# Kernel optimization log

Hardware: AMD Instinct MI355X
Metric: run time of the kernel (lower is better)

The kernel has to match this reference:

```python
import jax, jax.numpy as jnp
import numpy as np

EPS = 1e-4      # MovingBatchNorm eps
STEPS = 3       # fixed RK4 steps standing in for adaptive dopri5
B, N, D, C, H = 4, 2048, 3, 64, 512


def setup_inputs() -> dict:
    key = jax.random.key(0)
    ks = iter(jax.random.split(key, 40))
    f32 = jnp.float32

    def rn(shape, s=1.0):
        return jax.random.normal(next(ks), shape, dtype=f32) * s

    inp = {}
    inp['x'] = rn((B, N, D))
    inp['c'] = rn((B, N, C))
    for p in ('bn1', 'bn2'):
        inp[p + '_mean'] = rn((D,), 0.1)
        inp[p + '_var'] = jax.random.uniform(next(ks), (D,), dtype=f32, minval=0.5, maxval=1.5)
        inp[p + '_log_gamma'] = jnp.zeros((D,), f32)
        inp[p + '_beta'] = jnp.zeros((D,), f32)
    inp['sqrt_T'] = jnp.array([np.sqrt(0.5)], f32)  # train_T: T = sqrt_T**2
    dims = [(D, H), (H, H), (H, H), (H, D)]  # concatsquash (in, out)
    for i, (din, dout) in enumerate(dims):
        inp[f'W{i}'] = rn((dout, din), 0.05)
        inp[f'b{i}'] = jnp.zeros((dout,), f32)
        inp[f'Wg{i}'] = rn((dout, C + 1), 0.05)
        inp[f'bg{i}'] = jnp.zeros((dout,), f32)
        inp[f'Wb{i}'] = rn((dout, C + 1), 0.05)
    return inp


def _odenet(t, x, c, layers):
    # ConcatSquash MLP: lin(x)*sigmoid(hyper_gate([t,c])) + hyper_bias([t,c])
    ctx = jnp.concatenate([jnp.broadcast_to(t, c.shape[:-1] + (1,)).astype(x.dtype), c], axis=-1)
    h = x
    for i, (W, b, Wg, bg, Wb) in enumerate(layers):
        h = (h @ W.T + b) * jax.nn.sigmoid(ctx @ Wg.T + bg) + ctx @ Wb.T
        if i < len(layers) - 1:
            h = jnp.tanh(h)
    return h


def _aug_dyn(t, x, c, layers):
    # augmented CNF dynamics: (dx/dt, dlogp/dt) with exact divergence via D jvps
    f = lambda xx: _odenet(t, xx, c, layers)
    div = jnp.zeros(x.shape[:-1] + (1,), x.dtype)
    dx = None
    for i in range(x.shape[-1]):
        e = jnp.zeros_like(x).at[..., i].set(1.0)
        dx, jv = jax.jvp(f, (x,), (e,))
        div = div + jv[..., i:i + 1]
    return dx, -div


def _rk4(x0, lp0, c, layers, T):
    dt = T / STEPS

    def step(carry, i):
        x, lp = carry
        t = i.astype(x.dtype) * dt
        k1x, k1l = _aug_dyn(t, x, c, layers)
        k2x, k2l = _aug_dyn(t + 0.5 * dt, x + 0.5 * dt * k1x, c, layers)
        k3x, k3l = _aug_dyn(t + 0.5 * dt, x + 0.5 * dt * k2x, c, layers)
        k4x, k4l = _aug_dyn(t + dt, x + dt * k3x, c, layers)
        x = x + (dt / 6.0) * (k1x + 2.0 * k2x + 2.0 * k3x + k4x)
        lp = lp + (dt / 6.0) * (k1l + 2.0 * k2l + 2.0 * k3l + k4l)
        return (x, lp), None

    (x, lp), _ = jax.lax.scan(step, (x0, lp0), jnp.arange(STEPS))
    return x, lp


def _bn(x, lp, mean, var, log_gamma, beta):
    # MovingBatchNorm1d, eval mode; logdet = sum(log_gamma - 0.5*log(var+eps))
    y = (x - mean) * jnp.exp(log_gamma) / jnp.sqrt(var + EPS) + beta
    ld = jnp.sum(log_gamma - 0.5 * jnp.log(var + EPS))
    return y, lp - ld


def reference(x, c, bn1_mean, bn1_var, bn1_log_gamma, bn1_beta,
              bn2_mean, bn2_var, bn2_log_gamma, bn2_beta, sqrt_T,
              W0, b0, Wg0, bg0, Wb0, W1, b1, Wg1, bg1, Wb1,
              W2, b2, Wg2, bg2, Wb2, W3, b3, Wg3, bg3, Wb3):
    layers = [(W0, b0, Wg0, bg0, Wb0), (W1, b1, Wg1, bg1, Wb1),
              (W2, b2, Wg2, bg2, Wb2), (W3, b3, Wg3, bg3, Wb3)]
    lp = jnp.zeros(x.shape[:-1] + (1,), x.dtype)  # (B,N,1)
    x, lp = _bn(x, lp, bn1_mean, bn1_var, bn1_log_gamma, bn1_beta)
    T = sqrt_T[0] ** 2
    x, lp = _rk4(x, lp, c, layers, T)
    x, lp = _bn(x, lp, bn2_mean, bn2_var, bn2_log_gamma, bn2_beta)
    return x, jnp.sum(lp, axis=(1, 2))
```

## Files before the change

### kernel.cpp

```cpp
#include <hip/hip_runtime.h>
#include <hip/hip_fp8.h>

#define PTS 8192
#define HDIM 512
#define BN_EPS 1e-4f
#define HSTRB 528
#define TS 256.0f

typedef unsigned short u16;
typedef unsigned char u8;
typedef long long i64;
typedef u16 u16x8 __attribute__((ext_vector_type(8)));
typedef short s16x8 __attribute__((ext_vector_type(8)));
typedef float f32x4 __attribute__((ext_vector_type(4)));
typedef float f32x2 __attribute__((ext_vector_type(2)));

__device__ __forceinline__ float bf2f(u16 u) {
  unsigned x = ((unsigned)u) << 16;
  return __builtin_bit_cast(float, x);
}
__device__ __forceinline__ u16 f2bf(float f) {
  unsigned x = __builtin_bit_cast(unsigned, f);
  x += 0x7fffu + ((x >> 16) & 1u);
  return (u16)(x >> 16);
}
__device__ __forceinline__ u8 f2f8(float x) {
  int v = __builtin_amdgcn_cvt_pk_fp8_f32(x, x, 0, false);
  return (u8)(v & 0xff);
}
__device__ __forceinline__ unsigned pk4_f8(float a, float b, float c, float d) {
  int v = __builtin_amdgcn_cvt_pk_fp8_f32(a, b, 0, false);
  v = __builtin_amdgcn_cvt_pk_fp8_f32(c, d, v, true);
  return (unsigned)v;
}
__device__ __forceinline__ float sigf(float x) {
  return __builtin_amdgcn_rcpf(1.f + __expf(-x));
}
__device__ __forceinline__ float fast_tanh(float x) {
  float e = __expf(2.f * x);
  return 1.f - 2.f * __builtin_amdgcn_rcpf(e + 1.f);
}
__device__ __forceinline__ void gl2lds16(const u16* g, u16* l) {
  __builtin_amdgcn_global_load_lds(
      (const __attribute__((address_space(1))) void*)g,
      (__attribute__((address_space(3))) void*)l, 16, 0, 0);
}

struct PrepArgs {
  const float *W1, *W2;
  u8 *W1s, *W2s;
  const float* c;
  u16* cb;
  const float *Wg0, *Wg1, *Wg2, *Wb0, *Wb1, *Wb2;
  const float *bg0, *bg1, *bg2;
  u16* Wpack;
  float* bias_pack;
  const float *x, *m1, *v1, *lg1, *be1;
  float *x_cur, *lp_state;
  const float *Wg3, *bg3, *Wb3;
  float *G3, *B3;
  const float *W0, *b0, *b1, *b2, *W3;
  float *E0, *E1, *E2;
};
__global__ void prep_kernel(PrepArgs a) {
  int i = blockIdx.x * 256 + threadIdx.x;
  if (i < 512 * 512) {
    int n = i >> 9, k = i & 511;
    int c = k >> 5, kin = k & 31, q = kin >> 3, b = kin & 7;
    int w = n >> 6, nin = n & 63, j = nin >> 4, lr = nin & 15;
    size_t d = ((((size_t)(c * 8 + w) * 4 + j) * 64) + (q * 16 + lr)) * 8 + b;
    a.W1s[d] = f2f8(a.W1[i]);
    a.W2s[d] = f2f8(a.W2[i]);
  }
  if (i < PTS * 64) a.cb[i] = f2bf(a.c[i]);
  if (i < 6 * 512 * 64) {
    int sec = i >> 15;
    int within = i & 32767;
    int o = within >> 6, k = within & 63;
    const float* src[6] = {a.Wg0, a.Wg1, a.Wg2, a.Wb0, a.Wb1, a.Wb2};
    a.Wpack[i] = f2bf(src[sec][o * 65 + 1 + k]);
  }
  if (i < 3072) {
    int sec = i >> 9, o = i & 511;
    const float* bgl[3] = {a.bg0, a.bg1, a.bg2};
    a.bias_pack[i] = (sec < 3) ? bgl[sec][o] : 0.f;
  }
  if (i < 512) {
    int o = i;
    a.E0[o * 8 + 0] = a.W0[o * 3];
    a.E0[o * 8 + 1] = a.W0[o * 3 + 1];
    a.E0[o * 8 + 2] = a.W0[o * 3 + 2];
    a.E0[o * 8 + 3] = a.b0[o];
    a.E0[o * 8 + 4] = a.Wg0[o * 65];
    a.E0[o * 8 + 5] = a.Wb0[o * 65];
    a.E0[o * 8 + 6] = 0.f; a.E0[o * 8 + 7] = 0.f;
    a.E1[o * 4 + 0] = a.b1[o];
    a.E1[o * 4 + 1] = a.Wg1[o * 65];
    a.E1[o * 4 + 2] = a.Wb1[o * 65];
    a.E1[o * 4 + 3] = 0.f;
    a.E2[o * 8 + 0] = a.b2[o];
    a.E2[o * 8 + 1] = a.Wg2[o * 65];
    a.E2[o * 8 + 2] = a.Wb2[o * 65];
    a.E2[o * 8 + 3] = a.W3[o];
    a.E2[o * 8 + 4] = a.W3[512 + o];
    a.E2[o * 8 + 5] = a.W3[1024 + o];
    a.E2[o * 8 + 6] = 0.f; a.E2[o * 8 + 7] = 0.f;
  }
  if (i < PTS * 3) {
    int d = i % 3;
    a.x_cur[i] = (a.x[i] - a.m1[d]) * __expf(a.lg1[d]) * rsqrtf(a.v1[d] + BN_EPS) + a.be1[d];
  }
  if (i < PTS) a.lp_state[i] = 0.f;
  {
    int lane = threadIdx.x & 63;
    int p = (blockIdx.x * 256 + threadIdx.x) >> 6;
    float cv = a.c[(size_t)p * 64 + lane];
    float ag[3], ab[3];
    #pragma unroll
    for (int o = 0; o < 3; ++o) {
      ag[o] = cv * a.Wg3[o * 65 + 1 + lane];
      ab[o] = cv * a.Wb3[o * 65 + 1 + lane];
    }
    #pragma unroll
    for (int off = 32; off > 0; off >>= 1) {
      #pragma unroll
      for (int o = 0; o < 3; ++o) {
        ag[o] += __shfl_xor(ag[o], off);
        ab[o] += __shfl_xor(ab[o], off);
      }
    }
    if (lane == 0) {
      #pragma unroll
      for (int o = 0; o < 3; ++o) {
        a.G3[p * 3 + o] = ag[o] + a.bg3[o];
        a.B3[p * 3 + o] = ab[o];
      }
    }
  }
}

struct GatesGemmArgs {
  const u16 *A, *W;
  const float* bias;
  u16* GBi;
};
__global__ __launch_bounds__(256) void gates_gemm(GatesGemmArgs a) {
  __shared__ u16 As[128 * 32];
  __shared__ u16 Bs[128 * 32];
  int tid = threadIdx.x;
  int m0 = blockIdx.x * 128, n0 = blockIdx.y * 128;
  int wave = tid >> 6, lane = tid & 63;
  int wm = (wave & 1) * 64, wn = (wave >> 1) * 64;
  int lr = lane & 15, quad = lane >> 4;

  int rowS = tid >> 2, colS = (tid & 3) * 8;
  const u16* gA0 = a.A + (size_t)(m0 + rowS) * 64 + colS;
  const u16* gB0 = a.W + (size_t)(n0 + rowS) * 64 + colS;
  u16* sA0 = &As[tid * 8];
  u16* sA1 = &As[2048 + tid * 8];
  u16* sB0 = &Bs[tid * 8];
  u16* sB1 = &Bs[2048 + tid * 8];

  f32x4 acc[4][4];
  #pragma unroll
  for (int i = 0; i < 4; ++i)
    #pragma unroll
    for (int j = 0; j < 4; ++j)
      #pragma unroll
      for (int r = 0; r < 4; ++r) acc[i][j][r] = 0.f;

  for (int k0 = 0; k0 < 64; k0 += 32) {
    if (k0) __syncthreads();
    gl2lds16(gA0 + k0, sA0);
    gl2lds16(gA0 + (size_t)64 * 64 + k0, sA1);
    gl2lds16(gB0 + k0, sB0);
    gl2lds16(gB0 + (size_t)64 * 64 + k0, sB1);
    __syncthreads();
    s16x8 af[4], bfr[4];
    #pragma unroll
    for (int i = 0; i < 4; ++i)
      af[i] = *(const s16x8*)&As[(wm + i * 16 + lr) * 32 + quad * 8];
    #pragma unroll
    for (int j = 0; j < 4; ++j)
      bfr[j] = *(const s16x8*)&Bs[(wn + j * 16 + lr) * 32 + quad * 8];
    #pragma unroll
    for (int i = 0; i < 4; ++i)
      #pragma unroll
      for (int j = 0; j < 4; ++j)
        acc[i][j] = __builtin_amdgcn_mfma_f32_16x16x32_bf16(af[i], bfr[j], acc[i][j], 0, 0, 0);
  }

  #pragma unroll
  for (int j = 0; j < 4; ++j) {
    int n = n0 + wn + j * 16 + lr;
    int sec = n >> 9, col = n & 511;
    int l = (sec < 3) ? sec : sec - 3;
    int off = col * 2 + ((sec < 3) ? 0 : 1);
    float bv = a.bias[n];
    u16* outp = a.GBi + (size_t)l * PTS * 1024 + off;
    #pragma unroll
    for (int i = 0; i < 4; ++i) {
      int mrow = m0 + wm + i * 16 + quad * 4;
      #pragma unroll
      for (int r = 0; r < 4; ++r)
        outp[(size_t)(mrow + r) * 1024] = f2bf(acc[i][j][r] + bv);
    }
  }
}

struct StageArgs {
  const float* sqrtT;
  float ts_prev, ts_cur;
  int mode_prev;
  float* accum6;
  const float *G3, *B3, *Wg3, *Wb3, *b3;
  float *x_cur, *kx, *kl, *lp_state;
  const u16 *GBi0, *GBi1, *GBi2;
  const float *E0, *E1, *E2;
  const u8 *W1s, *W2s;
};

__global__ __launch_bounds__(512, 4) void stage_kernel(StageArgs a) {
  __shared__ __align__(16) u8 Hs[64 * HSTRB];
  __shared__ float xe[16][3];
  __shared__ float part[8][16][6];
  int tid = threadIdx.x;
  int w = tid >> 6, lane = tid & 63, lr = lane & 15, quad = lane >> 4;
  int n0 = w * 64;
  int p0 = blockIdx.x * 16;
  float s0 = a.sqrtT[0];
  float dt = s0 * s0 * (1.f / 3.f);

  const u8* w1l = a.W1s + (size_t)w * 2048 + (size_t)lane * 8;
  const u8* w2l = a.W2s + (size_t)w * 2048 + (size_t)lane * 8;

  i64 bc[4], bn[4];
  #pragma unroll
  for (int j = 0; j < 4; ++j) bc[j] = *(const i64*)(w1l + (size_t)j * 512);

  int pl0 = tid >> 5;
  int base_o = (tid & 31) * 16;
  const u16* g0row = a.GBi0 + (size_t)(p0 + pl0) * 1024 + 2 * base_o;
  u16x8 gc0 = *(const u16x8*)(g0row);
  u16x8 gc1 = *(const u16x8*)(g0row + 8);
  u16x8 gc2 = *(const u16x8*)(g0row + 16);
  u16x8 gc3 = *(const u16x8*)(g0row + 24);

  if (tid < 16) {
    int p = p0 + tid;
    float xc0 = a.x_cur[p * 3], xc1 = a.x_cur[p * 3 + 1], xc2 = a.x_cur[p * 3 + 2];
    float o0 = xc0, o1 = xc1, o2 = xc2;
    if (a.mode_prev >= 0) {
      float tp = a.ts_prev * dt;
      float dx[3], gate[3];
      #pragma unroll
      for (int r = 0; r < 3; ++r) {
        float fr = a.accum6[(size_t)p * 6 + r];
        gate[r] = sigf(a.G3[p * 3 + r] + tp * a.Wg3[r * 65]);
        float bias = a.B3[p * 3 + r] + tp * a.Wb3[r * 65];
        dx[r] = fmaf(fr + a.b3[r], gate[r], bias);
      }
      float klv = -(a.accum6[(size_t)p * 6 + 3] * gate[0] +
                    a.accum6[(size_t)p * 6 + 4] * gate[1] +
                    a.accum6[(size_t)p * 6 + 5] * gate[2]);
      int m = a.mode_prev;
      if (m == 0) {
        o0 = xc0 + 0.5f * dt * dx[0]; o1 = xc1 + 0.5f * dt * dx[1]; o2 = xc2 + 0.5f * dt * dx[2];
        a.kx[p * 3] = dx[0]; a.kx[p * 3 + 1] = dx[1]; a.kx[p * 3 + 2] = dx[2];
        a.kl[p] = klv;
      } else if (m == 1) {
        o0 = xc0 + 0.5f * dt * dx[0]; o1 = xc1 + 0.5f * dt * dx[1]; o2 = xc2 + 0.5f * dt * dx[2];
        a.kx[p * 3] += 2.f * dx[0]; a.kx[p * 3 + 1] += 2.f * dx[1]; a.kx[p * 3 + 2] += 2.f * dx[2];
        a.kl[p] += 2.f * klv;
      } else if (m == 2) {
        o0 = xc0 + dt * dx[0]; o1 = xc1 + dt * dx[1]; o2 = xc2 + dt * dx[2];
        a.kx[p * 3] += 2.f * dx[0]; a.kx[p * 3 + 1] += 2.f * dx[1]; a.kx[p * 3 + 2] += 2.f * dx[2];
        a.kl[p] += 2.f * klv;
      } else {
        float sc = dt * (1.f / 6.f);
        o0 = xc0 + sc * (a.kx[p * 3] + dx[0]);
        o1 = xc1 + sc * (a.kx[p * 3 + 1] + dx[1]);
        o2 = xc2 + sc * (a.kx[p * 3 + 2] + dx[2]);
        a.x_cur[p * 3] = o0; a.x_cur[p * 3 + 1] = o1; a.x_cur[p * 3 + 2] = o2;
        a.lp_state[p] += sc * (a.kl[p] + klv);
      }
    }
    xe[tid][0] = o0; xe[tid][1] = o1; xe[tid][2] = o2;
  }
  __syncthreads();

  float t = a.ts_cur * dt;

  {
    float x0 = xe[pl0][0], x1 = xe[pl0][1], x2 = xe[pl0][2];
    u16x8 gcv[4] = {gc0, gc1, gc2, gc3};
    #pragma unroll
    for (int cc = 0; cc < 4; ++cc) {
      u16x8 v = gcv[cc];
      float hk[4], d0k[4], d1k[4], d2k[4];
      #pragma unroll
      for (int k = 0; k < 4; ++k) {
        int o = base_o + cc * 4 + k;
        f32x4 e = *(const f32x4*)(a.E0 + (size_t)o * 8);
        f32x2 e2 = *(const f32x2*)(a.E0 + (size_t)o * 8 + 4);
        float u = fmaf(e[0], x0, fmaf(e[1], x1, e[2] * x2)) + e[3];
        float gate = sigf(bf2f(v[2 * k]) + t * e2[0]);
        float bias = bf2f(v[2 * k + 1]) + t * e2[1];
        float z = fmaf(u, gate, bias);
        float h = fast_tanh(z);
        float wm = (1.f - h * h) * gate * TS;
        hk[k] = h;
        d0k[k] = wm * e[0];
        d1k[k] = wm * e[1];
        d2k[k] = wm * e[2];
      }
      size_t hb = (size_t)(pl0 * 4) * HSTRB + base_o + cc * 4;
      *(unsigned*)(Hs + hb) = pk4_f8(hk[0], hk[1], hk[2], hk[3]);
      *(unsigned*)(Hs + hb + HSTRB) = pk4_f8(d0k[0], d0k[1], d0k[2], d0k[3]);
      *(unsigned*)(Hs + hb + 2 * HSTRB) = pk4_f8(d1k[0], d1k[1], d1k[2], d1k[3]);
      *(unsigned*)(Hs + hb + 3 * HSTRB) = pk4_f8(d2k[0], d2k[1], d2k[2], d2k[3]);
    }
  }

  unsigned g1v[4][4];
  #pragma unroll
  for (int j = 0; j < 4; ++j)
    #pragma unroll
    for (int i = 0; i < 4; ++i) {
      int n = n0 + j * 16 + lr;
      int p = p0 + i * 4 + quad;
      g1v[j][i] = *(const unsigned*)(a.GBi1 + (size_t)p * 1024 + 2 * n);
    }
  __syncthreads();

  f32x4 acc[4][4];
  #pragma unroll
  for (int i = 0; i < 4; ++i)
    #pragma unroll
    for (int j = 0; j < 4; ++j)
      #pragma unroll
      for (int r = 0; r < 4; ++r) acc[i][j][r] = 0.f;
  {
    #pragma unroll 1
    for (int c = 0; c < 16; ++c) {
      const u8* nsrc = (c < 15) ? (w1l + (size_t)(c + 1) * 16384) : w2l;
      #pragma unroll
      for (int j = 0; j < 4; ++j) bn[j] = *(const i64*)(nsrc + (size_t)j * 512);
      int k0 = c * 32;
      i64 af[4];
      #pragma unroll
      for (int i = 0; i < 4; ++i)
        af[i] = *(const i64*)(Hs + (size_t)(i * 16 + lr) * HSTRB + k0 + quad * 8);
      #pragma unroll
      for (int i = 0; i < 4; ++i)
        #pragma unroll
        for (int j = 0; j < 4; ++j)
          acc[i][j] = __builtin_amdgcn_mfma_f32_16x16x32_fp8_fp8(af[i], bc[j], acc[i][j], 0, 0, 0);
      #pragma unroll
      for (int j = 0; j < 4; ++j) bc[j] = bn[j];
    }
  }
  __syncthreads();

  #pragma unroll
  for (int j = 0; j < 4; ++j) {
    int n = n0 + j * 16 + lr;
    f32x4 e1 = *(const f32x4*)(a.E1 + (size_t)n * 4);
    #pragma unroll
    for (int i = 0; i < 4; ++i) {
      unsigned d = g1v[j][i];
      float gate = sigf(bf2f((u16)(d & 0xffffu)) + t * e1[1]);
      float bias = bf2f((u16)(d >> 16)) + t * e1[2];
      f32x4 u = acc[i][j];
      float z = fmaf(u[0] + e1[0], gate, bias);
      float h = fast_tanh(z);
      float wmf = (1.f - h * h) * gate;
      int row = i * 16 + quad * 4;
      Hs[(size_t)row * HSTRB + n] = f2f8(h);
      Hs[(size_t)(row + 1) * HSTRB + n] = f2f8(u[1] * wmf);
      Hs[(size_t)(row + 2) * HSTRB + n] = f2f8(u[2] * wmf);
      Hs[(size_t)(row + 3) * HSTRB + n] = f2f8(u[3] * wmf);
    }
  }

  unsigned g2v[4][4];
  #pragma unroll
  for (int j = 0; j < 4; ++j)
    #pragma unroll
    for (int i = 0; i < 4; ++i) {
      int n = n0 + j * 16 + lr;
      int p = p0 + i * 4 + quad;
      g2v[j][i] = *(const unsigned*)(a.GBi2 + (size_t)p * 1024 + 2 * n);
    }
  __syncthreads();

  #pragma unroll
  for (int i = 0; i < 4; ++i)
    #pragma unroll
    for (int j = 0; j < 4; ++j)
      #pragma unroll
      for (int r = 0; r < 4; ++r) acc[i][j][r] = 0.f;
  {
    #pragma unroll 1
    for (int c = 0; c < 16; ++c) {
      if (c < 15) {
        const u8* nsrc = w2l + (size_t)(c + 1) * 16384;
        #pragma unroll
        for (int j = 0; j < 4; ++j) bn[j] = *(const i64*)(nsrc + (size_t)j * 512);
      }
      int k0 = c * 32;
      i64 af[4];
      #pragma unroll
      for (int i = 0; i < 4; ++i)
        af[i] = *(const i64*)(Hs + (size_t)(i * 16 + lr) * HSTRB + k0 + quad * 8);
      #pragma unroll
      for (int i = 0; i < 4; ++i)
        #pragma unroll
        for (int j = 0; j < 4; ++j)
          acc[i][j] = __builtin_amdgcn_mfma_f32_16x16x32_fp8_fp8(af[i], bc[j], acc[i][j], 0, 0, 0);
      if (c < 15) {
        #pragma unroll
        for (int j = 0; j < 4; ++j) bc[j] = bn[j];
      }
    }
  }

  #pragma unroll
  for (int i = 0; i < 4; ++i) {
    float v0 = 0.f, v1 = 0.f, v2 = 0.f, v3 = 0.f, v4 = 0.f, v5 = 0.f;
    int pl = i * 4 + quad;
    #pragma unroll
    for (int j = 0; j < 4; ++j) {
      int n = n0 + j * 16 + lr;
      f32x4 ea = *(const f32x4*)(a.E2 + (size_t)n * 8);
      f32x2 eb = *(const f32x2*)(a.E2 + (size_t)n * 8 + 4);
      unsigned d = g2v[j][i];
      float gate = sigf(bf2f((u16)(d & 0xffffu)) + t * ea[1]);
      float bias = bf2f((u16)(d >> 16)) + t * ea[2];
      f32x4 u = acc[i][j];
      float z = fmaf(u[0] + ea[0], gate, bias);
      float h = fast_tanh(z);
      float wmf = (1.f - h * h) * gate;
      float w30 = ea[3], w31 = eb[0], w32 = eb[1];
      v0 = fmaf(h, w30, v0);
      v1 = fmaf(h, w31, v1);
      v2 = fmaf(h, w32, v2);
      v3 = fmaf(u[1] * wmf, w30, v3);
      v4 = fmaf(u[2] * wmf, w31, v4);
      v5 = fmaf(u[3] * wmf, w32, v5);
    }
    #pragma unroll
    for (int mask = 1; mask <= 8; mask <<= 1) {
      v0 += __shfl_xor(v0, mask);
      v1 += __shfl_xor(v1, mask);
      v2 += __shfl_xor(v2, mask);
      v3 += __shfl_xor(v3, mask);
      v4 += __shfl_xor(v4, mask);
      v5 += __shfl_xor(v5, mask);
    }
    float val = (lr == 0) ? v0 : (lr == 1) ? v1 : (lr == 2) ? v2
              : (lr == 3) ? v3 * (1.f / TS) : (lr == 4) ? v4 * (1.f / TS)
              : v5 * (1.f / TS);
    if (lr < 6) part[w][pl][lr] = val;
  }
  __syncthreads();

  if (tid < 96) {
    int pt = tid / 6, d = tid - pt * 6;
    float sum = 0.f;
    #pragma unroll
    for (int ww = 0; ww < 8; ++ww) sum += part[ww][pt][d];
    a.accum6[(size_t)(p0 + pt) * 6 + d] = sum;
  }
}

struct FinArgs {
  const float* sqrtT;
  const float* accum6;
  const float *G3, *B3, *Wg3, *Wb3, *b3;
  float *x_cur, *kx, *kl, *lp_state;
  const float *m2, *v2, *lg2, *be2;
  float* out_x;
};
__global__ void finalize_kernel(FinArgs a) {
  int p = blockIdx.x * 256 + threadIdx.x;
  if (p >= PTS) return;
  float s0 = a.sqrtT[0];
  float dt = s0 * s0 * (1.f / 3.f);
  float tp = 3.f * dt;
  float dx[3], gate[3];
  #pragma unroll
  for (int r = 0; r < 3; ++r) {
    float fr = a.accum6[(size_t)p * 6 + r];
    gate[r] = sigf(a.G3[p * 3 + r] + tp * a.Wg3[r * 65]);
    float bias = a.B3[p * 3 + r] + tp * a.Wb3[r * 65];
    dx[r] = fmaf(fr + a.b3[r], gate[r], bias);
  }
  float klv = -(a.accum6[(size_t)p * 6 + 3] * gate[0] +
                a.accum6[(size_t)p * 6 + 4] * gate[1] +
                a.accum6[(size_t)p * 6 + 5] * gate[2]);
  float sc = dt * (1.f / 6.f);
  #pragma unroll
  for (int r = 0; r < 3; ++r) {
    float xf = a.x_cur[p * 3 + r] + sc * (a.kx[p * 3 + r] + dx[r]);
    a.out_x[p * 3 + r] = (xf - a.m2[r]) * __expf(a.lg2[r]) * rsqrtf(a.v2[r] + BN_EPS) + a.be2[r];
  }
  a.lp_state[p] += sc * (a.kl[p] + klv);
}

__global__ void finish_lp(const float* __restrict__ lp_state,
                          const float* __restrict__ v1, const float* __restrict__ lg1,
                          const float* __restrict__ v2, const float* __restrict__ lg2,
                          float* __restrict__ out) {
  int b = blockIdx.x, tid = threadIdx.x;
  float s = 0.f;
  for (int n = tid; n < 2048; n += 256) s += lp_state[b * 2048 + n];
  __shared__ float red[256];
  red[tid] = s;
  __syncthreads();
  for (int w = 128; w > 0; w >>= 1) {
    if (tid < w) red[tid] += red[tid + w];
    __syncthreads();
  }
  if (tid == 0) {
    float ld = 0.f;
    for (int d = 0; d < 3; ++d) {
      ld += lg1[d] - 0.5f * logf(v1[d] + BN_EPS);
      ld += lg2[d] - 0.5f * logf(v2[d] + BN_EPS);
    }
    out[b] = red[0] - 2048.f * ld;
  }
}

extern "C" void kernel_launch(void* const* d_in, const int* in_sizes, int n_in,
                              void* d_out, int out_size, void* d_ws, size_t ws_size,
                              hipStream_t stream) {
  const float* x        = (const float*)d_in[0];
  const float* c        = (const float*)d_in[1];
  const float* bn1_mean = (const float*)d_in[2];
  const float* bn1_var  = (const float*)d_in[3];
  const float* bn1_lg   = (const float*)d_in[4];
  const float* bn1_beta = (const float*)d_in[5];
  const float* bn2_mean = (const float*)d_in[6];
  const float* bn2_var  = (const float*)d_in[7];
  const float* bn2_lg   = (const float*)d_in[8];
  const float* bn2_beta = (const float*)d_in[9];
  const float* sqrtT    = (const float*)d_in[10];
  const float* W0  = (const float*)d_in[11];
  const float* b0  = (const float*)d_in[12];
  const float* Wg0 = (const float*)d_in[13];
  const float* bg0 = (const float*)d_in[14];
  const float* Wb0 = (const float*)d_in[15];
  const float* W1  = (const float*)d_in[16];
  const float* b1  = (const float*)d_in[17];
  const float* Wg1 = (const float*)d_in[18];
  const float* bg1 = (const float*)d_in[19];
  const float* Wb1 = (const float*)d_in[20];
  const float* W2  = (const float*)d_in[21];
  const float* b2  = (const float*)d_in[22];
  const float* Wg2 = (const float*)d_in[23];
  const float* bg2 = (const float*)d_in[24];
  const float* Wb2 = (const float*)d_in[25];
  const float* W3  = (const float*)d_in[26];
  const float* b3  = (const float*)d_in[27];
  const float* Wg3 = (const float*)d_in[28];
  const float* bg3 = (const float*)d_in[29];
  const float* Wb3 = (const float*)d_in[30];

  char* base = (char*)d_ws;
  size_t off = 0;
  auto alloc = [&](size_t bytes) -> void* {
    void* pp = base + off;
    off += (bytes + 255) & ~(size_t)255;
    return pp;
  };
  u8* W1s = (u8*)alloc((size_t)512 * 512);
  u8* W2s = (u8*)alloc((size_t)512 * 512);
  u16* cb  = (u16*)alloc((size_t)PTS * 64 * 2);
  u16* Wpack = (u16*)alloc((size_t)6 * 512 * 64 * 2);
  float* bias_pack = (float*)alloc((size_t)3072 * 4);
  u16* GBi = (u16*)alloc((size_t)3 * PTS * 1024 * 2);
  const size_t SZi = (size_t)PTS * 1024;
  u16* GBi0 = GBi;
  u16* GBi1 = GBi + SZi;
  u16* GBi2 = GBi + 2 * SZi;
  float* G3f = (float*)alloc((size_t)PTS * 3 * 4);
  float* B3f = (float*)alloc((size_t)PTS * 3 * 4);
  float* E0 = (float*)alloc((size_t)512 * 8 * 4);
  float* E1 = (float*)alloc((size_t)512 * 4 * 4);
  float* E2 = (float*)alloc((size_t)512 * 8 * 4);
  float* accum6   = (float*)alloc((size_t)PTS * 6 * 4);
  float* x_cur    = (float*)alloc((size_t)PTS * 3 * 4);
  float* kx       = (float*)alloc((size_t)PTS * 3 * 4);
  float* kl       = (float*)alloc((size_t)PTS * 4);
  float* lp_state = (float*)alloc((size_t)PTS * 4);
  (void)ws_size; (void)in_sizes; (void)n_in; (void)out_size;

  PrepArgs pa{W1, W2, W1s, W2s, c, cb, Wg0, Wg1, Wg2, Wb0, Wb1, Wb2,
              bg0, bg1, bg2, Wpack, bias_pack, x, bn1_mean, bn1_var,
              bn1_lg, bn1_beta, x_cur, lp_state, Wg3, bg3, Wb3, G3f, B3f,
              W0, b0, b1, b2, W3, E0, E1, E2};
  prep_kernel<<<2048, 256, 0, stream>>>(pa);

  GatesGemmArgs gg{cb, Wpack, bias_pack, GBi};
  gates_gemm<<<dim3(64, 24), 256, 0, stream>>>(gg);

  auto ts_of = [](int s) -> float {
    static const float frac[4] = {0.f, 0.5f, 0.5f, 1.f};
    return (float)(s >> 2) + frac[s & 3];
  };

  for (int s = 0; s < 12; ++s) {
    StageArgs sa{sqrtT, (s == 0) ? 0.f : ts_of(s - 1), ts_of(s),
                 (s == 0) ? -1 : ((s - 1) & 3), accum6,
                 G3f, B3f, Wg3, Wb3, b3, x_cur, kx, kl, lp_state,
                 GBi0, GBi1, GBi2, E0, E1, E2, W1s, W2s};
    stage_kernel<<<PTS / 16, 512, 0, stream>>>(sa);
  }

  FinArgs fa{sqrtT, accum6, G3f, B3f, Wg3, Wb3, b3, x_cur, kx, kl,
             lp_state, bn2_mean, bn2_var, bn2_lg, bn2_beta, (float*)d_out};
  finalize_kernel<<<32, 256, 0, stream>>>(fa);
  finish_lp<<<4, 256, 0, stream>>>(lp_state, bn1_var, bn1_lg, bn2_var, bn2_lg,
                                   (float*)d_out + PTS * 3);
}
```

Before: 562.3 us.

## Fuse all RK4 stages into one persistent kernel using MX-scaled fp8 MFMA

Replaces the twelve stage launches and the finalize kernel with a single flow kernel. Each block keeps its 16 points' RK state (x, k-accumulators, logp) in shared memory across all 12 stages, which removes the per-stage global round-trips and launch gaps. The hidden-layer GEMMs switch from 16x16x32 fp8 MFMA to the scaled 16x16x128 f8f6f4 MFMA with unit scales, and W1/W2 are repacked to match, cutting instruction count per K chunk. In exchange, the persistent loop adds extra __syncthreads per stage, holds a larger register footprint for the 32-byte weight fragments, and re-reads the layer-0 gate data from global memory on every stage.

```diff
diff --git a/kernel.cpp b/kernel.cpp
--- a/kernel.cpp
+++ b/kernel.cpp
@@ -6,6 +6,7 @@
 #define BN_EPS 1e-4f
 #define HSTRB 528
 #define TS 256.0f
+#define SCL1 0x7f7f7f7f
 
 typedef unsigned short u16;
 typedef unsigned char u8;
@@ -14,6 +15,8 @@
 typedef short s16x8 __attribute__((ext_vector_type(8)));
 typedef float f32x4 __attribute__((ext_vector_type(4)));
 typedef float f32x2 __attribute__((ext_vector_type(2)));
+typedef int i32x4 __attribute__((ext_vector_type(4)));
+typedef int i32x8 __attribute__((ext_vector_type(8)));
 
 __device__ __forceinline__ float bf2f(u16 u) {
   unsigned x = ((unsigned)u) << 16;
@@ -56,7 +59,7 @@
   u16* Wpack;
   float* bias_pack;
   const float *x, *m1, *v1, *lg1, *be1;
-  float *x_cur, *lp_state;
+  float *x_cur;
   const float *Wg3, *bg3, *Wb3;
   float *G3, *B3;
   const float *W0, *b0, *b1, *b2, *W3;
@@ -66,9 +69,10 @@
   int i = blockIdx.x * 256 + threadIdx.x;
   if (i < 512 * 512) {
     int n = i >> 9, k = i & 511;
-    int c = k >> 5, kin = k & 31, q = kin >> 3, b = kin & 7;
-    int w = n >> 6, nin = n & 63, j = nin >> 4, lr = nin & 15;
-    size_t d = ((((size_t)(c * 8 + w) * 4 + j) * 64) + (q * 16 + lr)) * 8 + b;
+    int c = k >> 7, q2 = (k >> 5) & 3, b = k & 31;
+    int w = n >> 6, j = (n >> 4) & 3, lr = n & 15;
+    size_t d = (size_t)c * 65536 + (size_t)w * 8192 + (size_t)j * 2048 +
+               (size_t)(q2 * 16 + lr) * 32 + b;
     a.W1s[d] = f2f8(a.W1[i]);
     a.W2s[d] = f2f8(a.W2[i]);
   }
@@ -110,7 +114,6 @@
     int d = i % 3;
     a.x_cur[i] = (a.x[i] - a.m1[d]) * __expf(a.lg1[d]) * rsqrtf(a.v1[d] + BN_EPS) + a.be1[d];
   }
-  if (i < PTS) a.lp_state[i] = 0.f;
   {
     int lane = threadIdx.x & 63;
     int p = (blockIdx.x * 256 + threadIdx.x) >> 6;
@@ -208,22 +211,41 @@
   }
 }
 
-struct StageArgs {
+struct FlowArgs {
   const float* sqrtT;
-  float ts_prev, ts_cur;
-  int mode_prev;
-  float* accum6;
   const float *G3, *B3, *Wg3, *Wb3, *b3;
-  float *x_cur, *kx, *kl, *lp_state;
+  const float* x0;
   const u16 *GBi0, *GBi1, *GBi2;
   const float *E0, *E1, *E2;
   const u8 *W1s, *W2s;
+  const float *m2, *v2, *lg2, *be2;
+  float* out_x;
+  float* lp_state;
 };
 
-__global__ __launch_bounds__(512, 4) void stage_kernel(StageArgs a) {
+__device__ __forceinline__ void mx_chunk(const u8* hb, int c, f32x4 acc[4][4],
+                                         const i32x8 bw[4]) {
+  #pragma unroll
+  for (int i = 0; i < 4; ++i) {
+    const u8* ap = hb + (size_t)(i * 16) * HSTRB + c * 128;
+    i32x8 af;
+    *(i32x4*)&af = *(const i32x4*)ap;
+    *((i32x4*)&af + 1) = *(const i32x4*)(ap + 16);
+    #pragma unroll
+    for (int j = 0; j < 4; ++j)
+      acc[i][j] = __builtin_amdgcn_mfma_scale_f32_16x16x128_f8f6f4(
+          af, bw[j], acc[i][j], 0, 0, 0, SCL1, 0, SCL1);
+  }
+}
+
+__global__ __launch_bounds__(512, 4) void flow_kernel(FlowArgs a) {
   __shared__ __align__(16) u8 Hs[64 * HSTRB];
   __shared__ float xe[16][3];
   __shared__ float part[8][16][6];
+  __shared__ float xs[16][3], kxs[16][3];
+  __shared__ float kls[16], lps[16];
+  __shared__ float g3s[16][3], b3s[16][3];
+
   int tid = threadIdx.x;
   int w = tid >> 6, lane = tid & 63, lr = lane & 15, quad = lane >> 4;
   int n0 = w * 64;
@@ -231,281 +253,286 @@
   float s0 = a.sqrtT[0];
   float dt = s0 * s0 * (1.f / 3.f);
 
-  const u8* w1l = a.W1s + (size_t)w * 2048 + (size_t)lane * 8;
-  const u8* w2l = a.W2s + (size_t)w * 2048 + (size_t)lane * 8;
-
-  i64 bc[4], bn[4];
+  const u8* w1l = a.W1s + (size_t)w * 8192 + (size_t)lane * 32;
+  const u8* w2l = a.W2s + (size_t)w * 8192 + (size_t)lane * 32;
+  const u8* hb = (const u8*)Hs + (size_t)lr * HSTRB + quad * 32;
+
+  float wg3r[3], wb3r[3], b3r[3];
   #pragma unroll
-  for (int j = 0; j < 4; ++j) bc[j] = *(const i64*)(w1l + (size_t)j * 512);
+  for (int r = 0; r < 3; ++r) {
+    wg3r[r] = a.Wg3[r * 65];
+    wb3r[r] = a.Wb3[r * 65];
+    b3r[r] = a.b3[r];
+  }
+
+  if (tid < 16) {
+    int p = p0 + tid;
+    #pragma unroll
+    for (int r = 0; r < 3; ++r) {
+      xs[tid][r] = a.x0[p * 3 + r];
+      g3s[tid][r] = a.G3[p * 3 + r];
+      b3s[tid][r] = a.B3[p * 3 + r];
+    }
+    lps[tid] = 0.f;
+  }
 
   int pl0 = tid >> 5;
   int base_o = (tid & 31) * 16;
   const u16* g0row = a.GBi0 + (size_t)(p0 + pl0) * 1024 + 2 * base_o;
-  u16x8 gc0 = *(const u16x8*)(g0row);
-  u16x8 gc1 = *(const u16x8*)(g0row + 8);
-  u16x8 gc2 = *(const u16x8*)(g0row + 16);
-  u16x8 gc3 = *(const u16x8*)(g0row + 24);
+
+  #pragma unroll 1
+  for (int s = 0; s < 12; ++s) {
+    int sub = s & 3;
+    float ts_cur = (float)(s >> 2) + ((sub == 0) ? 0.f : (sub == 3) ? 1.f : 0.5f);
+
+    u16x8 gc0 = *(const u16x8*)(g0row);
+    u16x8 gc1 = *(const u16x8*)(g0row + 8);
+    u16x8 gc2 = *(const u16x8*)(g0row + 16);
+    u16x8 gc3 = *(const u16x8*)(g0row + 24);
+
+    __syncthreads();
+
+    if (tid < 16) {
+      float o0 = xs[tid][0], o1 = xs[tid][1], o2 = xs[tid][2];
+      if (s > 0) {
+        int m = (s - 1) & 3;
+        int psub = (s - 1) & 3;
+        float ts_prev = (float)((s - 1) >> 2) + ((psub == 0) ? 0.f : (psub == 3) ? 1.f : 0.5f);
+        float tp = ts_prev * dt;
+        float fr[6];
+        #pragma unroll
+        for (int r = 0; r < 6; ++r) {
+          float sum = part[0][tid][r];
+          #pragma unroll
+          for (int ww = 1; ww < 8; ++ww) sum += part[ww][tid][r];
+          fr[r] = sum;
+        }
+        float dx[3], gate[3];
+        #pragma unroll
+        for (int r = 0; r < 3; ++r) {
+          gate[r] = sigf(g3s[tid][r] + tp * wg3r[r]);
+          float bias = b3s[tid][r] + tp * wb3r[r];
+          dx[r] = fmaf(fr[r] + b3r[r], gate[r], bias);
+        }
+        float klv = -(fr[3] * gate[0] + fr[4] * gate[1] + fr[5] * gate[2]);
+        if (m == 0) {
+          o0 += 0.5f * dt * dx[0]; o1 += 0.5f * dt * dx[1]; o2 += 0.5f * dt * dx[2];
+          kxs[tid][0] = dx[0]; kxs[tid][1] = dx[1]; kxs[tid][2] = dx[2];
+          kls[tid] = klv;
+        } else if (m == 1) {
+          o0 += 0.5f * dt * dx[0]; o1 += 0.5f * dt * dx[1]; o2 += 0.5f * dt * dx[2];
+          kxs[tid][0] += 2.f * dx[0]; kxs[tid][1] += 2.f * dx[1]; kxs[tid][2] += 2.f * dx[2];
+          kls[tid] += 2.f * klv;
+        } else if (m == 2) {
+          o0 += dt * dx[0]; o1 += dt * dx[1]; o2 += dt * dx[2];
+          kxs[tid][0] += 2.f * dx[0]; kxs[tid][1] += 2.f * dx[1]; kxs[tid][2] += 2.f * dx[2];
+          kls[tid] += 2.f * klv;
+        } else {
+          float sc = dt * (1.f / 6.f);
+          o0 = xs[tid][0] + sc * (kxs[tid][0] + dx[0]);
+          o1 = xs[tid][1] + sc * (kxs[tid][1] + dx[1]);
+          o2 = xs[tid][2] + sc * (kxs[tid][2] + dx[2]);
+          xs[tid][0] = o0; xs[tid][1] = o1; xs[tid][2] = o2;
+          lps[tid] += sc * (kls[tid] + klv);
+        }
+      }
+      xe[tid][0] = o0; xe[tid][1] = o1; xe[tid][2] = o2;
+    }
+    __syncthreads();
+
+    float t = ts_cur * dt;
+
+    {
+      float x0v = xe[pl0][0], x1v = xe[pl0][1], x2v = xe[pl0][2];
+      u16x8 gcv[4] = {gc0, gc1, gc2, gc3};
+      #pragma unroll
+      for (int cc = 0; cc < 4; ++cc) {
+        u16x8 v = gcv[cc];
+        float hk[4], d0k[4], d1k[4], d2k[4];
+        #pragma unroll
+        for (int k = 0; k < 4; ++k) {
+          int o = base_o + cc * 4 + k;
+          f32x4 e = *(const f32x4*)(a.E0 + (size_t)o * 8);
+          f32x2 e2 = *(const f32x2*)(a.E0 + (size_t)o * 8 + 4);
+          float u = fmaf(e[0], x0v, fmaf(e[1], x1v, e[2] * x2v)) + e[3];
+          float gate = sigf(bf2f(v[2 * k]) + t * e2[0]);
+          float bias = bf2f(v[2 * k + 1]) + t * e2[1];
+          float z = fmaf(u, gate, bias);
+          float h = fast_tanh(z);
+          float wm = (1.f - h * h) * gate * TS;
+          hk[k] = h;
+          d0k[k] = wm * e[0];
+          d1k[k] = wm * e[1];
+          d2k[k] = wm * e[2];
+        }
+        size_t hbb = (size_t)(pl0 * 4) * HSTRB + base_o + cc * 4;
+        *(unsigned*)(Hs + hbb) = pk4_f8(hk[0], hk[1], hk[2], hk[3]);
+        *(unsigned*)(Hs + hbb + HSTRB) = pk4_f8(d0k[0], d0k[1], d0k[2], d0k[3]);
+        *(unsigned*)(Hs + hbb + 2 * HSTRB) = pk4_f8(d1k[0], d1k[1], d1k[2], d1k[3]);
+        *(unsigned*)(Hs + hbb + 3 * HSTRB) = pk4_f8(d2k[0], d2k[1], d2k[2], d2k[3]);
+      }
+    }
+
+    i32x8 bw[4];
+    #pragma unroll
+    for (int j = 0; j < 4; ++j) bw[j] = *(const i32x8*)(w1l + (size_t)j * 2048);
+
+    __syncthreads();
+
+    f32x4 acc[4][4];
+    #pragma unroll
+    for (int i = 0; i < 4; ++i)
+      #pragma unroll
+      for (int j = 0; j < 4; ++j)
+        #pragma unroll
+        for (int r = 0; r < 4; ++r) acc[i][j][r] = 0.f;
+
+    #pragma unroll 1
+    for (int c = 0; c < 3; ++c) {
+      __builtin_amdgcn_s_setprio(1);
+      mx_chunk(hb, c, acc, bw);
+      __builtin_amdgcn_s_setprio(0);
+      const u8* np = w1l + (size_t)(c + 1) * 65536;
+      #pragma unroll
+      for (int j = 0; j < 4; ++j) bw[j] = *(const i32x8*)(np + (size_t)j * 2048);
+    }
+    unsigned g1v[4][4];
+    #pragma unroll
+    for (int j = 0; j < 4; ++j)
+      #pragma unroll
+      for (int i = 0; i < 4; ++i)
+        g1v[j][i] = *(const unsigned*)(a.GBi1 + (size_t)(p0 + i * 4 + quad) * 1024 +
+                                       2 * (n0 + j * 16 + lr));
+    __builtin_amdgcn_s_setprio(1);
+    mx_chunk(hb, 3, acc, bw);
+    __builtin_amdgcn_s_setprio(0);
+    bw[0] = *(const i32x8*)(w2l);
+    bw[1] = *(const i32x8*)(w2l + 2048);
+
+    __syncthreads();
+
+    #pragma unroll
+    for (int j = 0; j < 4; ++j) {
+      int n = n0 + j * 16 + lr;
+      f32x4 e1 = *(const f32x4*)(a.E1 + (size_t)n * 4);
+      #pragma unroll
+      for (int i = 0; i < 4; ++i) {
+        unsigned d = g1v[j][i];
+        float gate = sigf(bf2f((u16)(d & 0xffffu)) + t * e1[1]);
+        float bias = bf2f((u16)(d >> 16)) + t * e1[2];
+        f32x4 u = acc[i][j];
+        float z = fmaf(u[0] + e1[0], gate, bias);
+        float h = fast_tanh(z);
+        float wmf = (1.f - h * h) * gate;
+        int row = i * 16 + quad * 4;
+        Hs[(size_t)row * HSTRB + n] = f2f8(h);
+        Hs[(size_t)(row + 1) * HSTRB + n] = f2f8(u[1] * wmf);
+        Hs[(size_t)(row + 2) * HSTRB + n] = f2f8(u[2] * wmf);
+        Hs[(size_t)(row + 3) * HSTRB + n] = f2f8(u[3] * wmf);
+      }
+    }
+    bw[2] = *(const i32x8*)(w2l + 4096);
+    bw[3] = *(const i32x8*)(w2l + 6144);
+
+    __syncthreads();
+
+    #pragma unroll
+    for (int i = 0; i < 4; ++i)
+      #pragma unroll
+      for (int j = 0; j < 4; ++j)
+        #pragma unroll
+        for (int r = 0; r < 4; ++r) acc[i][j][r] = 0.f;
+
+    #pragma unroll 1
+    for (int c = 0; c < 3; ++c) {
+      __builtin_amdgcn_s_setprio(1);
+      mx_chunk(hb, c, acc, bw);
+      __builtin_amdgcn_s_setprio(0);
+      const u8* np = w2l + (size_t)(c + 1) * 65536;
+      #pragma unroll
+      for (int j = 0; j < 4; ++j) bw[j] = *(const i32x8*)(np + (size_t)j * 2048);
+    }
+    unsigned g2v[4][4];
+    #pragma unroll
+    for (int j = 0; j < 4; ++j)
+      #pragma unroll
+      for (int i = 0; i < 4; ++i)
+        g2v[j][i] = *(const unsigned*)(a.GBi2 + (size_t)(p0 + i * 4 + quad) * 1024 +
+                                       2 * (n0 + j * 16 + lr));
+    __builtin_amdgcn_s_setprio(1);
+    mx_chunk(hb, 3, acc, bw);
+    __builtin_amdgcn_s_setprio(0);
+
+    #pragma unroll
+    for (int i = 0; i < 4; ++i) {
+      float v0 = 0.f, v1 = 0.f, v2 = 0.f, v3 = 0.f, v4 = 0.f, v5 = 0.f;
+      int pl = i * 4 + quad;
+      #pragma unroll
+      for (int j = 0; j < 4; ++j) {
+        int n = n0 + j * 16 + lr;
+        f32x4 ea = *(const f32x4*)(a.E2 + (size_t)n * 8);
+        f32x2 eb = *(const f32x2*)(a.E2 + (size_t)n * 8 + 4);
+        unsigned d = g2v[j][i];
+        float gate = sigf(bf2f((u16)(d & 0xffffu)) + t * ea[1]);
+        float bias = bf2f((u16)(d >> 16)) + t * ea[2];
+        f32x4 u = acc[i][j];
+        float z = fmaf(u[0] + ea[0], gate, bias);
+        float h = fast_tanh(z);
+        float wmf = (1.f - h * h) * gate;
+        float w30 = ea[3], w31 = eb[0], w32 = eb[1];
+        v0 = fmaf(h, w30, v0);
+        v1 = fmaf(h, w31, v1);
+        v2 = fmaf(h, w32, v2);
+        v3 = fmaf(u[1] * wmf, w30, v3);
+        v4 = fmaf(u[2] * wmf, w31, v4);
+        v5 = fmaf(u[3] * wmf, w32, v5);
+      }
+      #pragma unroll
+      for (int mask = 1; mask <= 8; mask <<= 1) {
+        v0 += __shfl_xor(v0, mask);
+        v1 += __shfl_xor(v1, mask);
+        v2 += __shfl_xor(v2, mask);
+        v3 += __shfl_xor(v3, mask);
+        v4 += __shfl_xor(v4, mask);
+        v5 += __shfl_xor(v5, mask);
+      }
+      float val = (lr == 0) ? v0 : (lr == 1) ? v1 : (lr == 2) ? v2
+                : (lr == 3) ? v3 * (1.f / TS) : (lr == 4) ? v4 * (1.f / TS)
+                : v5 * (1.f / TS);
+      if (lr < 6) part[w][pl][lr] = val;
+    }
+  }
+
+  __syncthreads();
 
   if (tid < 16) {
     int p = p0 + tid;
-    float xc0 = a.x_cur[p * 3], xc1 = a.x_cur[p * 3 + 1], xc2 = a.x_cur[p * 3 + 2];
-    float o0 = xc0, o1 = xc1, o2 = xc2;
-    if (a.mode_prev >= 0) {
-      float tp = a.ts_prev * dt;
-      float dx[3], gate[3];
-      #pragma unroll
-      for (int r = 0; r < 3; ++r) {
-        float fr = a.accum6[(size_t)p * 6 + r];
-        gate[r] = sigf(a.G3[p * 3 + r] + tp * a.Wg3[r * 65]);
-        float bias = a.B3[p * 3 + r] + tp * a.Wb3[r * 65];
-        dx[r] = fmaf(fr + a.b3[r], gate[r], bias);
-      }
-      float klv = -(a.accum6[(size_t)p * 6 + 3] * gate[0] +
-                    a.accum6[(size_t)p * 6 + 4] * gate[1] +
-                    a.accum6[(size_t)p * 6 + 5] * gate[2]);
-      int m = a.mode_prev;
-      if (m == 0) {
-        o0 = xc0 + 0.5f * dt * dx[0]; o1 = xc1 + 0.5f * dt * dx[1]; o2 = xc2 + 0.5f * dt * dx[2];
-        a.kx[p * 3] = dx[0]; a.kx[p * 3 + 1] = dx[1]; a.kx[p * 3 + 2] = dx[2];
-        a.kl[p] = klv;
-      } else if (m == 1) {
-        o0 = xc0 + 0.5f * dt * dx[0]; o1 = xc1 + 0.5f * dt * dx[1]; o2 = xc2 + 0.5f * dt * dx[2];
-        a.kx[p * 3] += 2.f * dx[0]; a.kx[p * 3 + 1] += 2.f * dx[1]; a.kx[p * 3 + 2] += 2.f * dx[2];
-        a.kl[p] += 2.f * klv;
-      } else if (m == 2) {
-        o0 = xc0 + dt * dx[0]; o1 = xc1 + dt * dx[1]; o2 = xc2 + dt * dx[2];
-        a.kx[p * 3] += 2.f * dx[0]; a.kx[p * 3 + 1] += 2.f * dx[1]; a.kx[p * 3 + 2] += 2.f * dx[2];
-        a.kl[p] += 2.f * klv;
-      } else {
-        float sc = dt * (1.f / 6.f);
-        o0 = xc0 + sc * (a.kx[p * 3] + dx[0]);
-        o1 = xc1 + sc * (a.kx[p * 3 + 1] + dx[1]);
-        o2 = xc2 + sc * (a.kx[p * 3 + 2] + dx[2]);
-        a.x_cur[p * 3] = o0; a.x_cur[p * 3 + 1] = o1; a.x_cur[p * 3 + 2] = o2;
-        a.lp_state[p] += sc * (a.kl[p] + klv);
-      }
-    }
-    xe[tid][0] = o0; xe[tid][1] = o1; xe[tid][2] = o2;
-  }
-  __syncthreads();
-
-  float t = a.ts_cur * dt;
-
-  {
-    float x0 = xe[pl0][0], x1 = xe[pl0][1], x2 = xe[pl0][2];
-    u16x8 gcv[4] = {gc0, gc1, gc2, gc3};
-    #pragma unroll
-    for (int cc = 0; cc < 4; ++cc) {
-      u16x8 v = gcv[cc];
-      float hk[4], d0k[4], d1k[4], d2k[4];
-      #pragma unroll
-      for (int k = 0; k < 4; ++k) {
-        int o = base_o + cc * 4 + k;
-        f32x4 e = *(const f32x4*)(a.E0 + (size_t)o * 8);
-        f32x2 e2 = *(const f32x2*)(a.E0 + (size_t)o * 8 + 4);
-        float u = fmaf(e[0], x0, fmaf(e[1], x1, e[2] * x2)) + e[3];
-        float gate = sigf(bf2f(v[2 * k]) + t * e2[0]);
-        float bias = bf2f(v[2 * k + 1]) + t * e2[1];
-        float z = fmaf(u, gate, bias);
-        float h = fast_tanh(z);
-        float wm = (1.f - h * h) * gate * TS;
-        hk[k] = h;
-        d0k[k] = wm * e[0];
-        d1k[k] = wm * e[1];
-        d2k[k] = wm * e[2];
-      }
-      size_t hb = (size_t)(pl0 * 4) * HSTRB + base_o + cc * 4;
-      *(unsigned*)(Hs + hb) = pk4_f8(hk[0], hk[1], hk[2], hk[3]);
-      *(unsigned*)(Hs + hb + HSTRB) = pk4_f8(d0k[0], d0k[1], d0k[2], d0k[3]);
-      *(unsigned*)(Hs + hb + 2 * HSTRB) = pk4_f8(d1k[0], d1k[1], d1k[2], d1k[3]);
-      *(unsigned*)(Hs + hb + 3 * HSTRB) = pk4_f8(d2k[0], d2k[1], d2k[2], d2k[3]);
-    }
-  }
-
-  unsigned g1v[4][4];
-  #pragma unroll
-  for (int j = 0; j < 4; ++j)
-    #pragma unroll
-    for (int i = 0; i < 4; ++i) {
-      int n = n0 + j * 16 + lr;
-      int p = p0 + i * 4 + quad;
-      g1v[j][i] = *(const unsigned*)(a.GBi1 + (size_t)p * 1024 + 2 * n);
-    }
-  __syncthreads();
-
-  f32x4 acc[4][4];
-  #pragma unroll
-  for (int i = 0; i < 4; ++i)
-    #pragma unroll
-    for (int j = 0; j < 4; ++j)
-      #pragma unroll
-      for (int r = 0; r < 4; ++r) acc[i][j][r] = 0.f;
-  {
-    #pragma unroll 1
-    for (int c = 0; c < 16; ++c) {
-      const u8* nsrc = (c < 15) ? (w1l + (size_t)(c + 1) * 16384) : w2l;
-      #pragma unroll
-      for (int j = 0; j < 4; ++j) bn[j] = *(const i64*)(nsrc + (size_t)j * 512);
-      int k0 = c * 32;
-      i64 af[4];
-      #pragma unroll
-      for (int i = 0; i < 4; ++i)
-        af[i] = *(const i64*)(Hs + (size_t)(i * 16 + lr) * HSTRB + k0 + quad * 8);
-      #pragma unroll
-      for (int i = 0; i < 4; ++i)
-        #pragma unroll
-        for (int j = 0; j < 4; ++j)
-          acc[i][j] = __builtin_amdgcn_mfma_f32_16x16x32_fp8_fp8(af[i], bc[j], acc[i][j], 0, 0, 0);
-      #pragma unroll
-      for (int j = 0; j < 4; ++j) bc[j] = bn[j];
-    }
-  }
-  __syncthreads();
-
-  #pragma unroll
-  for (int j = 0; j < 4; ++j) {
-    int n = n0 + j * 16 + lr;
-    f32x4 e1 = *(const f32x4*)(a.E1 + (size_t)n * 4);
-    #pragma unroll
-    for (int i = 0; i < 4; ++i) {
-      unsigned d = g1v[j][i];
-      float gate = sigf(bf2f((u16)(d & 0xffffu)) + t * e1[1]);
-      float bias = bf2f((u16)(d >> 16)) + t * e1[2];
-      f32x4 u = acc[i][j];
-      float z = fmaf(u[0] + e1[0], gate, bias);
-      float h = fast_tanh(z);
-      float wmf = (1.f - h * h) * gate;
-      int row = i * 16 + quad * 4;
-      Hs[(size_t)row * HSTRB + n] = f2f8(h);
-      Hs[(size_t)(row + 1) * HSTRB + n] = f2f8(u[1] * wmf);
-      Hs[(size_t)(row + 2) * HSTRB + n] = f2f8(u[2] * wmf);
-      Hs[(size_t)(row + 3) * HSTRB + n] = f2f8(u[3] * wmf);
-    }
-  }
-
-  unsigned g2v[4][4];
-  #pragma unroll
-  for (int j = 0; j < 4; ++j)
-    #pragma unroll
-    for (int i = 0; i < 4; ++i) {
-      int n = n0 + j * 16 + lr;
-      int p = p0 + i * 4 + quad;
-      g2v[j][i] = *(const unsigned*)(a.GBi2 + (size_t)p * 1024 + 2 * n);
-    }
-  __syncthreads();
-
-  #pragma unroll
-  for (int i = 0; i < 4; ++i)
-    #pragma unroll
-    for (int j = 0; j < 4; ++j)
-      #pragma unroll
-      for (int r = 0; r < 4; ++r) acc[i][j][r] = 0.f;
-  {
-    #pragma unroll 1
-    for (int c = 0; c < 16; ++c) {
-      if (c < 15) {
-        const u8* nsrc = w2l + (size_t)(c + 1) * 16384;
-        #pragma unroll
-        for (int j = 0; j < 4; ++j) bn[j] = *(const i64*)(nsrc + (size_t)j * 512);
-      }
-      int k0 = c * 32;
-      i64 af[4];
-      #pragma unroll
-      for (int i = 0; i < 4; ++i)
-        af[i] = *(const i64*)(Hs + (size_t)(i * 16 + lr) * HSTRB + k0 + quad * 8);
-      #pragma unroll
-      for (int i = 0; i < 4; ++i)
-        #pragma unroll
-        for (int j = 0; j < 4; ++j)
-          acc[i][j] = __builtin_amdgcn_mfma_f32_16x16x32_fp8_fp8(af[i], bc[j], acc[i][j], 0, 0, 0);
-      if (c < 15) {
-        #pragma unroll
-        for (int j = 0; j < 4; ++j) bc[j] = bn[j];
-      }
-    }
-  }
-
-  #pragma unroll
-  for (int i = 0; i < 4; ++i) {
-    float v0 = 0.f, v1 = 0.f, v2 = 0.f, v3 = 0.f, v4 = 0.f, v5 = 0.f;
-    int pl = i * 4 + quad;
-    #pragma unroll
-    for (int j = 0; j < 4; ++j) {
-      int n = n0 + j * 16 + lr;
-      f32x4 ea = *(const f32x4*)(a.E2 + (size_t)n * 8);
-      f32x2 eb = *(const f32x2*)(a.E2 + (size_t)n * 8 + 4);
-      unsigned d = g2v[j][i];
-      float gate = sigf(bf2f((u16)(d & 0xffffu)) + t * ea[1]);
-      float bias = bf2f((u16)(d >> 16)) + t * ea[2];
-      f32x4 u = acc[i][j];
-      float z = fmaf(u[0] + ea[0], gate, bias);
-      float h = fast_tanh(z);
-      float wmf = (1.f - h * h) * gate;
-      float w30 = ea[3], w31 = eb[0], w32 = eb[1];
-      v0 = fmaf(h, w30, v0);
-      v1 = fmaf(h, w31, v1);
-      v2 = fmaf(h, w32, v2);
-      v3 = fmaf(u[1] * wmf, w30, v3);
-      v4 = fmaf(u[2] * wmf, w31, v4);
-      v5 = fmaf(u[3] * wmf, w32, v5);
-    }
-    #pragma unroll
-    for (int mask = 1; mask <= 8; mask <<= 1) {
-      v0 += __shfl_xor(v0, mask);
-      v1 += __shfl_xor(v1, mask);
-      v2 += __shfl_xor(v2, mask);
-      v3 += __shfl_xor(v3, mask);
-      v4 += __shfl_xor(v4, mask);
-      v5 += __shfl_xor(v5, mask);
-    }
-    float val = (lr == 0) ? v0 : (lr == 1) ? v1 : (lr == 2) ? v2
-              : (lr == 3) ? v3 * (1.f / TS) : (lr == 4) ? v4 * (1.f / TS)
-              : v5 * (1.f / TS);
-    if (lr < 6) part[w][pl][lr] = val;
-  }
-  __syncthreads();
-
-  if (tid < 96) {
-    int pt = tid / 6, d = tid - pt * 6;
-    float sum = 0.f;
-    #pragma unroll
-    for (int ww = 0; ww < 8; ++ww) sum += part[ww][pt][d];
-    a.accum6[(size_t)(p0 + pt) * 6 + d] = sum;
-  }
-}
-
-struct FinArgs {
-  const float* sqrtT;
-  const float* accum6;
-  const float *G3, *B3, *Wg3, *Wb3, *b3;
-  float *x_cur, *kx, *kl, *lp_state;
-  const float *m2, *v2, *lg2, *be2;
-  float* out_x;
-};
-__global__ void finalize_kernel(FinArgs a) {
-  int p = blockIdx.x * 256 + threadIdx.x;
-  if (p >= PTS) return;
-  float s0 = a.sqrtT[0];
-  float dt = s0 * s0 * (1.f / 3.f);
-  float tp = 3.f * dt;
-  float dx[3], gate[3];
-  #pragma unroll
-  for (int r = 0; r < 3; ++r) {
-    float fr = a.accum6[(size_t)p * 6 + r];
-    gate[r] = sigf(a.G3[p * 3 + r] + tp * a.Wg3[r * 65]);
-    float bias = a.B3[p * 3 + r] + tp * a.Wb3[r * 65];
-    dx[r] = fmaf(fr + a.b3[r], gate[r], bias);
-  }
-  float klv = -(a.accum6[(size_t)p * 6 + 3] * gate[0] +
-                a.accum6[(size_t)p * 6 + 4] * gate[1] +
-                a.accum6[(size_t)p * 6 + 5] * gate[2]);
-  float sc = dt * (1.f / 6.f);
-  #pragma unroll
-  for (int r = 0; r < 3; ++r) {
-    float xf = a.x_cur[p * 3 + r] + sc * (a.kx[p * 3 + r] + dx[r]);
-    a.out_x[p * 3 + r] = (xf - a.m2[r]) * __expf(a.lg2[r]) * rsqrtf(a.v2[r] + BN_EPS) + a.be2[r];
-  }
-  a.lp_state[p] += sc * (a.kl[p] + klv);
+    float tp = 3.f * dt;
+    float fr[6];
+    #pragma unroll
+    for (int r = 0; r < 6; ++r) {
+      float sum = part[0][tid][r];
+      #pragma unroll
+      for (int ww = 1; ww < 8; ++ww) sum += part[ww][tid][r];
+      fr[r] = sum;
+    }
+    float dx[3], gate[3];
+    #pragma unroll
+    for (int r = 0; r < 3; ++r) {
+      gate[r] = sigf(g3s[tid][r] + tp * wg3r[r]);
+      float bias = b3s[tid][r] + tp * wb3r[r];
+      dx[r] = fmaf(fr[r] + b3r[r], gate[r], bias);
+    }
+    float klv = -(fr[3] * gate[0] + fr[4] * gate[1] + fr[5] * gate[2]);
+    float sc = dt * (1.f / 6.f);
+    #pragma unroll
+    for (int r = 0; r < 3; ++r) {
+      float xf = xs[tid][r] + sc * (kxs[tid][r] + dx[r]);
+      a.out_x[p * 3 + r] =
+          (xf - a.m2[r]) * __expf(a.lg2[r]) * rsqrtf(a.v2[r] + BN_EPS) + a.be2[r];
+    }
+    a.lp_state[p] = lps[tid] + sc * (kls[tid] + klv);
+  }
 }
 
 __global__ void finish_lp(const float* __restrict__ lp_state,
@@ -589,38 +616,24 @@
   float* E0 = (float*)alloc((size_t)512 * 8 * 4);
   float* E1 = (float*)alloc((size_t)512 * 4 * 4);
   float* E2 = (float*)alloc((size_t)512 * 8 * 4);
-  float* accum6   = (float*)alloc((size_t)PTS * 6 * 4);
   float* x_cur    = (float*)alloc((size_t)PTS * 3 * 4);
-  float* kx       = (float*)alloc((size_t)PTS * 3 * 4);
-  float* kl       = (float*)alloc((size_t)PTS * 4);
   float* lp_state = (float*)alloc((size_t)PTS * 4);
   (void)ws_size; (void)in_sizes; (void)n_in; (void)out_size;
 
   PrepArgs pa{W1, W2, W1s, W2s, c, cb, Wg0, Wg1, Wg2, Wb0, Wb1, Wb2,
               bg0, bg1, bg2, Wpack, bias_pack, x, bn1_mean, bn1_var,
-              bn1_lg, bn1_beta, x_cur, lp_state, Wg3, bg3, Wb3, G3f, B3f,
+              bn1_lg, bn1_beta, x_cur, Wg3, bg3, Wb3, G3f, B3f,
               W0, b0, b1, b2, W3, E0, E1, E2};
   prep_kernel<<<2048, 256, 0, stream>>>(pa);
 
   GatesGemmArgs gg{cb, Wpack, bias_pack, GBi};
   gates_gemm<<<dim3(64, 24), 256, 0, stream>>>(gg);
 
-  auto ts_of = [](int s) -> float {
-    static const float frac[4] = {0.f, 0.5f, 0.5f, 1.f};
-    return (float)(s >> 2) + frac[s & 3];
-  };
-
-  for (int s = 0; s < 12; ++s) {
-    StageArgs sa{sqrtT, (s == 0) ? 0.f : ts_of(s - 1), ts_of(s),
-                 (s == 0) ? -1 : ((s - 1) & 3), accum6,
-                 G3f, B3f, Wg3, Wb3, b3, x_cur, kx, kl, lp_state,
-                 GBi0, GBi1, GBi2, E0, E1, E2, W1s, W2s};
-    stage_kernel<<<PTS / 16, 512, 0, stream>>>(sa);
-  }
-
-  FinArgs fa{sqrtT, accum6, G3f, B3f, Wg3, Wb3, b3, x_cur, kx, kl,
-             lp_state, bn2_mean, bn2_var, bn2_lg, bn2_beta, (float*)d_out};
-  finalize_kernel<<<32, 256, 0, stream>>>(fa);
+  FlowArgs fa{sqrtT, G3f, B3f, Wg3, Wb3, b3, x_cur, GBi0, GBi1, GBi2,
+              E0, E1, E2, W1s, W2s, bn2_mean, bn2_var, bn2_lg, bn2_beta,
+              (float*)d_out, lp_state};
+  flow_kernel<<<PTS / 16, 512, 0, stream>>>(fa);
+
   finish_lp<<<4, 256, 0, stream>>>(lp_state, bn1_var, bn1_lg, bn2_var, bn2_lg,
                                    (float*)d_out + PTS * 3);
 }
```

Measured after the change: 865.5 us. +53.9%, slower.
